# Kernel optimization log

Hardware: AMD Instinct MI355X
Metric: run time of the kernel (lower is better)

## Reference

```python
import jax, jax.numpy as jnp
import numpy as np

USER_NUM = 100000
ITEM_NUM = 50000
N_EDGES = 2000000
EMB = 64
N_LAYERS = 3


def setup_inputs() -> dict:
    key = jax.random.key(0)
    k1, k2, k3, k4 = jax.random.split(key, 4)
    # xavier-uniform-like init scale for embeddings
    scale = float(np.sqrt(6.0 / (USER_NUM + EMB)))
    user_emb = jax.random.uniform(k1, (USER_NUM, EMB), jnp.float32, -scale, scale)
    scale_i = float(np.sqrt(6.0 / (ITEM_NUM + EMB)))
    item_emb = jax.random.uniform(k2, (ITEM_NUM, EMB), jnp.float32, -scale_i, scale_i)
    u_idx = jax.random.randint(k3, (N_EDGES,), 0, USER_NUM, jnp.int32)
    i_idx = jax.random.randint(k4, (N_EDGES,), 0, ITEM_NUM, jnp.int32)
    return {"user_emb": user_emb, "item_emb": item_emb, "u_idx": u_idx, "i_idx": i_idx}


def _degree_norms(u_idx, i_idx):
    ones = jnp.ones(u_idx.shape[0], jnp.float32)
    d_u = jax.ops.segment_sum(ones, u_idx, num_segments=USER_NUM)
    d_i = jax.ops.segment_sum(ones, i_idx, num_segments=ITEM_NUM)
    d_u = jnp.where(d_u == 0, 1.0, d_u)
    d_i = jnp.where(d_i == 0, 1.0, d_i)
    return ((1.0 / d_u)[:, None], (1.0 / d_i)[:, None],
            (d_u ** -0.5)[:, None], (d_i ** -0.5)[:, None])


def reference(user_emb, item_emb, u_idx, i_idx):
    d_u_inv, d_i_inv, d_u_inv_sqrt, d_i_inv_sqrt = _degree_norms(u_idx, i_idx)

    # SpMM via gather + segment_sum on the edge list (binary interaction values)
    def spmm_rt(x_u):  # (rt @ x_u): [U,D] -> [I,D]
        return jax.ops.segment_sum(x_u[u_idx], i_idx, num_segments=ITEM_NUM)

    def spmm_r(x_i):  # (r @ x_i): [I,D] -> [U,D]
        return jax.ops.segment_sum(x_i[i_idx], u_idx, num_segments=USER_NUM)

    user_e = user_emb
    item_e = item_emb
    sum_u = user_e
    sum_i = item_e
    for _ in range(N_LAYERS):
        # user propagation: u -> hyperedge(items) -> u
        tmp_u = user_e * d_u_inv_sqrt
        tmp_i = spmm_rt(tmp_u) * d_i_inv
        user_e = spmm_r(tmp_i) * d_u_inv_sqrt
        sum_u = sum_u + user_e
        # item propagation: i -> hyperedge(users) -> i
        tmp_i2 = item_e * d_i_inv_sqrt
        tmp_u2 = spmm_r(tmp_i2) * d_u_inv
        item_e = spmm_rt(tmp_u2) * d_i_inv_sqrt
        sum_i = sum_i + item_e
    inv = 1.0 / (N_LAYERS + 1)
    return sum_u * inv, sum_i * inv
```

## Files before the change

### kernel.cpp

```cpp
#include <hip/hip_runtime.h>
#include <hip/hip_fp16.h>
#include <math.h>

#define U_NUM 100000
#define I_NUM 50000
#define NE    2000000
#define EMB   64
#define NLAYERS 3

#define BSH   7
#define BROWS 128
#define NBU_U ((U_NUM + BROWS - 1) >> BSH)
#define NBU_I ((I_NUM + BROWS - 1) >> BSH)
#define NBU_T (NBU_U + NBU_I)
#define PACK_SH 17
#define PACK_MASK 0x1FFFF

#define CAP_U 4096
#define CAP_I 6144

#define CHUNK2 2048
#define NBLK2 ((NE + CHUNK2 - 1) / CHUNK2)

#define DBINS 512

#define ND_U ((U_NUM + 2047) / 2048)
#define ND_I ((I_NUM + 2047) / 2048)
#define NINIT (((U_NUM + I_NUM) * (EMB / 4) + 255) / 256)

#define FP8_SCALE 512.0f

typedef float v2f __attribute__((ext_vector_type(2)));

static inline int ceil_div(int a, int b){ return (a + b - 1) / b; }


__global__ void binfill_k(const int* __restrict__ u_idx, const int* __restrict__ i_idx,
                          int* __restrict__ bcur_u, int* __restrict__ bcur_i,
                          int* __restrict__ bin_u, int* __restrict__ bin_i){
  __shared__ int scnt[NBU_T];
  __shared__ int gbase[NBU_T];
  __shared__ int scur[NBU_T];
  int t = threadIdx.x;
  for (int k = t; k < NBU_T; k += 256){ scnt[k] = 0; scur[k] = 0; }
  __syncthreads();
  int e0 = blockIdx.x * CHUNK2 + t * 8;
  int u[8], iv[8];
  bool act = e0 < NE;
  if (act){
    int4 a = *(const int4*)(u_idx + e0);
    int4 b = *(const int4*)(u_idx + e0 + 4);
    int4 c = *(const int4*)(i_idx + e0);
    int4 d = *(const int4*)(i_idx + e0 + 4);
    u[0]=a.x; u[1]=a.y; u[2]=a.z; u[3]=a.w; u[4]=b.x; u[5]=b.y; u[6]=b.z; u[7]=b.w;
    iv[0]=c.x; iv[1]=c.y; iv[2]=c.z; iv[3]=c.w; iv[4]=d.x; iv[5]=d.y; iv[6]=d.z; iv[7]=d.w;
#pragma unroll
    for (int k = 0; k < 8; ++k){
      atomicAdd(&scnt[u[k] >> BSH], 1);
      atomicAdd(&scnt[NBU_U + (iv[k] >> BSH)], 1);
    }
  }
  __syncthreads();
  for (int k = t; k < NBU_T; k += 256){
    int c = scnt[k];
    if (c){
      int* bc = (k < NBU_U) ? (bcur_u + k) : (bcur_i + (k - NBU_U));
      gbase[k] = atomicAdd(bc, c);
    }
  }
  __syncthreads();
  if (act){
#pragma unroll
    for (int k = 0; k < 8; ++k){
      int bu = u[k] >> BSH;
      int p = atomicAdd(&scur[bu], 1);
      bin_u[(size_t)bu * CAP_U + gbase[bu] + p] =
          ((u[k] & (BROWS - 1)) << PACK_SH) | iv[k];
      int bi = NBU_U + (iv[k] >> BSH);
      int p2 = atomicAdd(&scur[bi], 1);
      bin_i[(size_t)(bi - NBU_U) * CAP_I + gbase[bi] + p2] =
          ((iv[k] & (BROWS - 1)) << PACK_SH) | u[k];
    }
  }
}

__global__ void small_scan2_k(const int* __restrict__ cA, int* __restrict__ oA,
                              int* __restrict__ rA, int nA,
                              const int* __restrict__ cB, int* __restrict__ oB,
                              int* __restrict__ rB, int nB){
  const int* cnt; int* offs; int* cur; int n;
  if (blockIdx.x == 0){ cnt = cA; offs = oA; cur = rA; n = nA; }
  else { cnt = cB; offs = oB; cur = rB; n = nB; }
  __shared__ int s[1024];
  int t = threadIdx.x;
  int v = (t < n) ? cnt[t] : 0;
  s[t] = v; __syncthreads();
  for (int o = 1; o < 1024; o <<= 1){
    int x = (t >= o) ? s[t - o] : 0;
    __syncthreads();
    s[t] += x;
    __syncthreads();
  }
  int excl = (t > 0) ? s[t - 1] : 0;
  if (t < n){ offs[t] = excl; cur[t] = excl; }
  if (t == n - 1) offs[n] = s[t];
}


__global__ void bucket_build_k(const int* __restrict__ bin_u, const int* __restrict__ bin_i,
                               const int* __restrict__ bcnt_u, const int* __restrict__ bcnt_i,
                               const int* __restrict__ boffs_u, const int* __restrict__ boffs_i,
                               int* __restrict__ cnt_u, int* __restrict__ cnt_i,
                               int* __restrict__ offs_u, int* __restrict__ offs_i,
                               float* __restrict__ du_inv, float* __restrict__ du_invs,
                               float* __restrict__ di_inv, float* __restrict__ di_invs,
                               int* __restrict__ adj_u, int* __restrict__ adj_i,
                               int* __restrict__ dhist_u, int* __restrict__ dhist_i){
  __shared__ int h[BROWS];
  __shared__ int part[256];
  __shared__ int dh[DBINS];
  int b = blockIdx.x;
  const int* bin; const int* bcnt; const int* boffs; int* cnt; int* offs;
  float* inv; float* invs; int* adj; int* dhist; int jj, nrows; size_t cap;
  if (b < NBU_U){
    bin = bin_u; bcnt = bcnt_u; boffs = boffs_u; cnt = cnt_u; offs = offs_u;
    inv = du_inv; invs = du_invs; adj = adj_u; dhist = dhist_u; jj = b; nrows = U_NUM; cap = CAP_U;
  } else {
    bin = bin_i; bcnt = bcnt_i; boffs = boffs_i; cnt = cnt_i; offs = offs_i;
    inv = di_inv; invs = di_invs; adj = adj_i; dhist = dhist_i; jj = b - NBU_U; nrows = I_NUM; cap = CAP_I;
  }
  int tid = threadIdx.x;
  int r0 = jj << BSH;
  const int* binb = bin + (size_t)jj * cap;
  int ne = bcnt[jj];
  int badj = boffs[jj];
  if (tid < BROWS) h[tid] = 0;
  for (int t = tid; t < DBINS; t += 256) dh[t] = 0;
  __syncthreads();
  for (int e = tid; e < ne; e += 256)
    atomicAdd(&h[((unsigned)binb[e]) >> PACK_SH], 1);
  __syncthreads();
  int c = (tid < BROWS) ? h[tid] : 0;
  part[tid] = c; __syncthreads();
  for (int o = 1; o < 256; o <<= 1){
    int x = (tid >= o) ? part[tid - o] : 0;
    __syncthreads();
    part[tid] += x;
    __syncthreads();
  }
  int excl = (tid > 0) ? part[tid - 1] : 0;
  if (tid < BROWS){
    h[tid] = excl;
    int row = r0 + tid;
    if (row < nrows){
      cnt[row] = c;
      offs[row] = badj + excl;
      float d = (c > 0) ? (float)c : 1.0f;
      inv[row]  = 1.0f / d;
      invs[row] = 1.0f / sqrtf(d);
      atomicAdd(&dh[min(c, DBINS - 1)], 1);
    } else if (row == nrows){
      offs[row] = badj + excl;
    }
  }
  __syncthreads();
  for (int e = tid; e < ne; e += 256){
    int v = binb[e];
    int slot = badj + atomicAdd(&h[((unsigned)v) >> PACK_SH], 1);
    adj[slot] = v & PACK_MASK;
  }
  __syncthreads();
  for (int t = tid; t < DBINS; t += 256) if (dh[t]) atomicAdd(&dhist[t], dh[t]);
}


__device__ __forceinline__ unsigned pack4_fp8(float a, float b, float c, float d){
  int p = 0;
  p = __builtin_amdgcn_cvt_pk_fp8_f32(a, b, p, false);
  p = __builtin_amdgcn_cvt_pk_fp8_f32(c, d, p, true);
  return (unsigned)p;
}

__device__ __forceinline__ void accq(float* a, uint2 q){
  v2f f0 = __builtin_amdgcn_cvt_pk_f32_fp8(q.x, false);
  v2f f1 = __builtin_amdgcn_cvt_pk_f32_fp8(q.x, true);
  v2f f2 = __builtin_amdgcn_cvt_pk_f32_fp8(q.y, false);
  v2f f3 = __builtin_amdgcn_cvt_pk_f32_fp8(q.y, true);
  a[0] += f0.x; a[1] += f0.y; a[2] += f1.x; a[3] += f1.y;
  a[4] += f2.x; a[5] += f2.y; a[6] += f3.x; a[7] += f3.y;
}


__global__ void post_k(const int* __restrict__ cnt_u, const int* __restrict__ offs_u,
                       const int* __restrict__ dhist_u, int* __restrict__ dcur_u,
                       int4* __restrict__ rd_u,
                       const int* __restrict__ cnt_i, const int* __restrict__ offs_i,
                       const int* __restrict__ dhist_i, int* __restrict__ dcur_i,
                       int4* __restrict__ rd_i,
                       const float* __restrict__ ue, const float* __restrict__ ie,
                       const float* __restrict__ dus, const float* __restrict__ dis,
                       float* __restrict__ out, unsigned char* __restrict__ u0,
                       unsigned char* __restrict__ i0){
  int b = blockIdx.x;
  int t = threadIdx.x;
  if (b >= ND_U + ND_I){
    int idx4 = (b - ND_U - ND_I) * 256 + t;
    const int nu4 = U_NUM * (EMB / 4);
    const int tot4 = (U_NUM + I_NUM) * (EMB / 4);
    if (idx4 >= tot4) return;
    const float* e; unsigned char* hp; float s; int loc;
    if (idx4 < nu4){ e = ue; hp = u0; loc = idx4; s = dus[idx4 >> 4] * FP8_SCALE; }
    else { e = ie; hp = i0; loc = idx4 - nu4; s = dis[(idx4 - nu4) >> 4] * FP8_SCALE; }
    float4 v = ((const float4*)e)[loc];
    ((float4*)out)[idx4] = make_float4(v.x * 0.25f, v.y * 0.25f, v.z * 0.25f, v.w * 0.25f);
    ((unsigned*)hp)[loc] = pack4_fp8(v.x * s, v.y * s, v.z * s, v.w * s);
    return;
  }
  const int* cnt; const int* offs; const int* dhist; int* dcur; int4* rd; int n, base;
  if (b < ND_U){ cnt = cnt_u; offs = offs_u; dhist = dhist_u; dcur = dcur_u; rd = rd_u; n = U_NUM; base = b * 2048; }
  else { cnt = cnt_i; offs = offs_i; dhist = dhist_i; dcur = dcur_i; rd = rd_i; n = I_NUM; base = (b - ND_U) * 2048; }
  __shared__ int sc[DBINS];
  __shared__ int h[DBINS];
  __shared__ int base_s[DBINS];
  sc[t] = dhist[t]; sc[t + 256] = dhist[t + 256];
  h[t] = 0; h[t + 256] = 0;
  __syncthreads();
  for (int o = 1; o < DBINS; o <<= 1){
    int x0 = (t >= o) ? sc[t - o] : 0;
    int x1 = ((t + 256) >= o) ? sc[t + 256 - o] : 0;
    __syncthreads();
    sc[t] += x0; sc[t + 256] += x1;
    __syncthreads();
  }
  int end = min(base + 2048, n);
  for (int r = base + t; r < end; r += 256)
    atomicAdd(&h[min(cnt[r], DBINS - 1)], 1);
  __syncthreads();
  for (int tt = t; tt < DBINS; tt += 256){
    int c = h[tt];
    int excl = tt ? sc[tt - 1] : 0;
    base_s[tt] = c ? (excl + atomicAdd(&dcur[tt], c)) : 0;
    h[tt] = 0;
  }
  __syncthreads();
  for (int r = base + t; r < end; r += 256){
    int c = cnt[r];
    int bb = min(c, DBINS - 1);
    int pos = base_s[bb] + atomicAdd(&h[bb], 1);
    int bg = offs[r];
    rd[n - 1 - pos] = make_int4(bg, bg + c, r, 0);
  }
}


__global__ void spmm_pair(
    const int4* __restrict__ rdA, const int* __restrict__ adjA,
    const unsigned char* __restrict__ srcA, const float* __restrict__ phA,
    unsigned char* __restrict__ dstA, int nA,
    const int4* __restrict__ rdB, const int* __restrict__ adjB,
    const unsigned char* __restrict__ srcB, const float* __restrict__ phB,
    unsigned char* __restrict__ dstB, int nB){
  int t = blockIdx.x * blockDim.x + threadIdx.x;
  int rid = t >> 3;
  int lane = t & 7;
  const int4* rd; const int* adj; const unsigned char* src; const float* ph;
  unsigned char* dst;
  if (rid < nA){
    rd = rdA; adj = adjA; src = srcA; ph = phA; dst = dstA;
  } else {
    rid -= nA;
    if (rid >= nB) return;
    rd = rdB; adj = adjB; src = srcB; ph = phB; dst = dstB;
  }
  int4 d = rd[rid];
  int beg = d.x, end = d.y, row = d.z;
  const unsigned char* sp8 = src + (size_t)(lane << 3);
  float acc[8];
#pragma unroll
  for (int k = 0; k < 8; ++k) acc[k] = 0.f;
  int j = beg;
  for (; j + 7 < end; j += 8){
    int n0 = adj[j],   n1 = adj[j+1], n2 = adj[j+2], n3 = adj[j+3];
    int n4 = adj[j+4], n5 = adj[j+5], n6 = adj[j+6], n7 = adj[j+7];
    uint2 q0 = *(const uint2*)(sp8 + (((size_t)n0) << 6));
    uint2 q1 = *(const uint2*)(sp8 + (((size_t)n1) << 6));
    uint2 q2 = *(const uint2*)(sp8 + (((size_t)n2) << 6));
    uint2 q3 = *(const uint2*)(sp8 + (((size_t)n3) << 6));
    uint2 q4 = *(const uint2*)(sp8 + (((size_t)n4) << 6));
    uint2 q5 = *(const uint2*)(sp8 + (((size_t)n5) << 6));
    uint2 q6 = *(const uint2*)(sp8 + (((size_t)n6) << 6));
    uint2 q7 = *(const uint2*)(sp8 + (((size_t)n7) << 6));
    accq(acc, q0); accq(acc, q1); accq(acc, q2); accq(acc, q3);
    accq(acc, q4); accq(acc, q5); accq(acc, q6); accq(acc, q7);
  }
  for (; j < end; ++j){
    int n0 = adj[j];
    uint2 q0 = *(const uint2*)(sp8 + (((size_t)n0) << 6));
    accq(acc, q0);
  }
  float phv = ph[row];
  unsigned lo = pack4_fp8(acc[0] * phv, acc[1] * phv, acc[2] * phv, acc[3] * phv);
  unsigned hi = pack4_fp8(acc[4] * phv, acc[5] * phv, acc[6] * phv, acc[7] * phv);
  *(uint2*)(dst + (((size_t)row) << 6) + (size_t)(lane << 3)) = make_uint2(lo, hi);
}


__global__ void merge_k(const unsigned char* __restrict__ u1, const unsigned char* __restrict__ u2,
                        const unsigned char* __restrict__ u3,
                        const unsigned char* __restrict__ i1, const unsigned char* __restrict__ i2,
                        const unsigned char* __restrict__ i3,
                        const float* __restrict__ du_inv, const float* __restrict__ du_invs,
                        const float* __restrict__ di_inv, const float* __restrict__ di_invs,
                        float* __restrict__ out){
  int idx4 = blockIdx.x * blockDim.x + threadIdx.x;
  const int nu4 = U_NUM * (EMB / 4);
  const int tot4 = (U_NUM + I_NUM) * (EMB / 4);
  if (idx4 >= tot4) return;
  const unsigned char *t1, *t2, *t3; float ratio; int loc;
  if (idx4 < nu4){
    t1 = u1; t2 = u2; t3 = u3; loc = idx4;
    int row = idx4 >> 4;
    ratio = (0.25f / FP8_SCALE) * du_invs[row] / du_inv[row];
  } else {
    loc = idx4 - nu4;
    t1 = i1; t2 = i2; t3 = i3;
    int row = loc >> 4;
    ratio = (0.25f / FP8_SCALE) * di_invs[row] / di_inv[row];
  }
  unsigned q1 = ((const unsigned*)t1)[loc];
  unsigned q2 = ((const unsigned*)t2)[loc];
  unsigned q3 = ((const unsigned*)t3)[loc];
  float4 o = ((float4*)out)[idx4];
  v2f a, b;
  a = __builtin_amdgcn_cvt_pk_f32_fp8(q1, false); b = __builtin_amdgcn_cvt_pk_f32_fp8(q1, true);
  o.x += ratio * a.x; o.y += ratio * a.y; o.z += ratio * b.x; o.w += ratio * b.y;
  a = __builtin_amdgcn_cvt_pk_f32_fp8(q2, false); b = __builtin_amdgcn_cvt_pk_f32_fp8(q2, true);
  o.x += ratio * a.x; o.y += ratio * a.y; o.z += ratio * b.x; o.w += ratio * b.y;
  a = __builtin_amdgcn_cvt_pk_f32_fp8(q3, false); b = __builtin_amdgcn_cvt_pk_f32_fp8(q3, true);
  o.x += ratio * a.x; o.y += ratio * a.y; o.z += ratio * b.x; o.w += ratio * b.y;
  ((float4*)out)[idx4] = o;
}


extern "C" void kernel_launch(void* const* d_in, const int* in_sizes, int n_in,
                              void* d_out, int out_size, void* d_ws, size_t ws_size,
                              hipStream_t stream){
  const float* user_emb = (const float*)d_in[0];
  const float* item_emb = (const float*)d_in[1];
  const int*   u_idx    = (const int*)d_in[2];
  const int*   i_idx    = (const int*)d_in[3];
  float* out = (float*)d_out;

  char* w = (char*)d_ws;
  size_t off = 0;
  auto alloc = [&](size_t bytes) -> void* {
    void* p = (void*)(w + off);
    off += (bytes + 255) & ~(size_t)255;
    return p;
  };
  int* zb      = (int*)alloc((size_t)(NBU_T + 4 * DBINS) * 4);
  int* bcur_u  = zb;
  int* bcur_i  = bcur_u + NBU_U;
  int* dhist_u = bcur_i + NBU_I;
  int* dhist_i = dhist_u + DBINS;
  int* dcur_u  = dhist_i + DBINS;
  int* dcur_i  = dcur_u + DBINS;
  int* boffs_u = (int*)alloc((size_t)(NBU_U + 1) * 4);
  int* boffs_i = (int*)alloc((size_t)(NBU_I + 1) * 4);
  int* scr_u   = (int*)alloc((size_t)NBU_U * 4);
  int* scr_i   = (int*)alloc((size_t)NBU_I * 4);
  int* cnt_u   = (int*)alloc((size_t)U_NUM * 4);
  int* cnt_i   = (int*)alloc((size_t)I_NUM * 4);
  int* offs_u  = (int*)alloc((size_t)(U_NUM + 1) * 4);
  int* offs_i  = (int*)alloc((size_t)(I_NUM + 1) * 4);
  int4* rd_u   = (int4*)alloc((size_t)U_NUM * 16);
  int4* rd_i   = (int4*)alloc((size_t)I_NUM * 16);
  int* adj_u   = (int*)alloc((size_t)NE * 4);
  int* adj_i   = (int*)alloc((size_t)NE * 4);
  float* du_inv  = (float*)alloc((size_t)U_NUM * 4);
  float* du_invs = (float*)alloc((size_t)U_NUM * 4);
  float* di_inv  = (float*)alloc((size_t)I_NUM * 4);
  float* di_invs = (float*)alloc((size_t)I_NUM * 4);
  const size_t URB = (size_t)U_NUM * EMB;
  const size_t IRB = (size_t)I_NUM * EMB;
  unsigned char* hreg = (unsigned char*)alloc(4 * URB + 4 * IRB + URB + IRB);
  unsigned char* u0 = hreg;
  unsigned char* u1 = u0 + URB;
  unsigned char* u2 = u1 + URB;
  unsigned char* u3 = u2 + URB;
  unsigned char* i0 = u3 + URB;
  unsigned char* i1 = i0 + IRB;
  unsigned char* i2 = i1 + IRB;
  unsigned char* i3 = i2 + IRB;
  unsigned char* tmp_i = i3 + IRB;
  unsigned char* tmp_u = tmp_i + IRB;
  int* bin_u = (int*)hreg;
  int* bin_i = bin_u + (size_t)NBU_U * CAP_U;

  hipMemsetAsync(zb, 0, (size_t)(NBU_T + 4 * DBINS) * 4, stream);
  binfill_k<<<NBLK2, 256, 0, stream>>>(u_idx, i_idx, bcur_u, bcur_i, bin_u, bin_i);
  small_scan2_k<<<2, 1024, 0, stream>>>(bcur_u, boffs_u, scr_u, NBU_U,
                                        bcur_i, boffs_i, scr_i, NBU_I);
  bucket_build_k<<<NBU_T, 256, 0, stream>>>(bin_u, bin_i, bcur_u, bcur_i,
                                            boffs_u, boffs_i,
                                            cnt_u, cnt_i, offs_u, offs_i,
                                            du_inv, du_invs, di_inv, di_invs,
                                            adj_u, adj_i, dhist_u, dhist_i);

  post_k<<<ND_U + ND_I + NINIT, 256, 0, stream>>>(
      cnt_u, offs_u, dhist_u, dcur_u, rd_u,
      cnt_i, offs_i, dhist_i, dcur_i, rd_i,
      user_emb, item_emb, du_invs, di_invs, out, u0, i0);

  const int pair_grid = ceil_div((U_NUM + I_NUM) * 8, 256);
  unsigned char* uls[4] = { u0, u1, u2, u3 };
  unsigned char* ils[4] = { i0, i1, i2, i3 };
  for (int l = 0; l < NLAYERS; ++l){
    spmm_pair<<<pair_grid, 256, 0, stream>>>(
        rd_i, adj_i, uls[l], di_inv, tmp_i, I_NUM,
        rd_u, adj_u, ils[l], du_inv, tmp_u, U_NUM);
    spmm_pair<<<pair_grid, 256, 0, stream>>>(
        rd_u, adj_u, tmp_i, du_inv, uls[l + 1], U_NUM,
        rd_i, adj_i, tmp_u, di_inv, ils[l + 1], I_NUM);
  }

  merge_k<<<NINIT, 256, 0, stream>>>(u1, u2, u3, i1, i2, i3,
                                     du_inv, du_invs, di_inv, di_invs, out);
}
```

Baseline: 492.1 us.

## Widen SpMM gathers to 16-byte loads with four lanes per row, enlarge binfill chunks

The SpMM kernel now assigns four threads per row, each loading 16 fp8 values with a uint4 gather instead of eight threads each loading 8 bytes. This halves the thread count and gives wider memory transactions, at the cost of more registers per thread (16 accumulators) and less parallelism across rows. Separately, the binning kernel processes 8192 edges per block in a loop and re-reads the indices on the second pass. This is meant to amortize the per-block shared-memory init and the global atomics on bin cursors.

```diff
diff --git a/kernel.cpp b/kernel.cpp
--- a/kernel.cpp
+++ b/kernel.cpp
@@ -19,7 +19,7 @@
 #define CAP_U 4096
 #define CAP_I 6144
 
-#define CHUNK2 2048
+#define CHUNK2 8192
 #define NBLK2 ((NE + CHUNK2 - 1) / CHUNK2)
 
 #define DBINS 512
@@ -44,21 +44,21 @@
   int t = threadIdx.x;
   for (int k = t; k < NBU_T; k += 256){ scnt[k] = 0; scur[k] = 0; }
   __syncthreads();
-  int e0 = blockIdx.x * CHUNK2 + t * 8;
-  int u[8], iv[8];
-  bool act = e0 < NE;
-  if (act){
+  int base = blockIdx.x * CHUNK2;
+  int end = min(base + CHUNK2, NE);
+  for (int e0 = base + t * 8; e0 < end; e0 += 2048){
     int4 a = *(const int4*)(u_idx + e0);
     int4 b = *(const int4*)(u_idx + e0 + 4);
     int4 c = *(const int4*)(i_idx + e0);
     int4 d = *(const int4*)(i_idx + e0 + 4);
-    u[0]=a.x; u[1]=a.y; u[2]=a.z; u[3]=a.w; u[4]=b.x; u[5]=b.y; u[6]=b.z; u[7]=b.w;
-    iv[0]=c.x; iv[1]=c.y; iv[2]=c.z; iv[3]=c.w; iv[4]=d.x; iv[5]=d.y; iv[6]=d.z; iv[7]=d.w;
-#pragma unroll
-    for (int k = 0; k < 8; ++k){
-      atomicAdd(&scnt[u[k] >> BSH], 1);
-      atomicAdd(&scnt[NBU_U + (iv[k] >> BSH)], 1);
-    }
+    atomicAdd(&scnt[a.x >> BSH], 1); atomicAdd(&scnt[a.y >> BSH], 1);
+    atomicAdd(&scnt[a.z >> BSH], 1); atomicAdd(&scnt[a.w >> BSH], 1);
+    atomicAdd(&scnt[b.x >> BSH], 1); atomicAdd(&scnt[b.y >> BSH], 1);
+    atomicAdd(&scnt[b.z >> BSH], 1); atomicAdd(&scnt[b.w >> BSH], 1);
+    atomicAdd(&scnt[NBU_U + (c.x >> BSH)], 1); atomicAdd(&scnt[NBU_U + (c.y >> BSH)], 1);
+    atomicAdd(&scnt[NBU_U + (c.z >> BSH)], 1); atomicAdd(&scnt[NBU_U + (c.w >> BSH)], 1);
+    atomicAdd(&scnt[NBU_U + (d.x >> BSH)], 1); atomicAdd(&scnt[NBU_U + (d.y >> BSH)], 1);
+    atomicAdd(&scnt[NBU_U + (d.z >> BSH)], 1); atomicAdd(&scnt[NBU_U + (d.w >> BSH)], 1);
   }
   __syncthreads();
   for (int k = t; k < NBU_T; k += 256){
@@ -69,7 +69,13 @@
     }
   }
   __syncthreads();
-  if (act){
+  for (int e0 = base + t * 8; e0 < end; e0 += 2048){
+    int4 a = *(const int4*)(u_idx + e0);
+    int4 b = *(const int4*)(u_idx + e0 + 4);
+    int4 c = *(const int4*)(i_idx + e0);
+    int4 d = *(const int4*)(i_idx + e0 + 4);
+    int u[8] = { a.x, a.y, a.z, a.w, b.x, b.y, b.z, b.w };
+    int iv[8] = { c.x, c.y, c.z, c.w, d.x, d.y, d.z, d.w };
 #pragma unroll
     for (int k = 0; k < 8; ++k){
       int bu = u[k] >> BSH;
@@ -181,13 +187,14 @@
   return (unsigned)p;
 }
 
-__device__ __forceinline__ void accq(float* a, uint2 q){
-  v2f f0 = __builtin_amdgcn_cvt_pk_f32_fp8(q.x, false);
-  v2f f1 = __builtin_amdgcn_cvt_pk_f32_fp8(q.x, true);
-  v2f f2 = __builtin_amdgcn_cvt_pk_f32_fp8(q.y, false);
-  v2f f3 = __builtin_amdgcn_cvt_pk_f32_fp8(q.y, true);
+__device__ __forceinline__ void accw(float* a, unsigned w){
+  v2f f0 = __builtin_amdgcn_cvt_pk_f32_fp8(w, false);
+  v2f f1 = __builtin_amdgcn_cvt_pk_f32_fp8(w, true);
   a[0] += f0.x; a[1] += f0.y; a[2] += f1.x; a[3] += f1.y;
-  a[4] += f2.x; a[5] += f2.y; a[6] += f3.x; a[7] += f3.y;
+}
+
+__device__ __forceinline__ void accq16(float* a, uint4 q){
+  accw(a, q.x); accw(a + 4, q.y); accw(a + 8, q.z); accw(a + 12, q.w);
 }
 
 
@@ -261,8 +268,8 @@
     const unsigned char* __restrict__ srcB, const float* __restrict__ phB,
     unsigned char* __restrict__ dstB, int nB){
   int t = blockIdx.x * blockDim.x + threadIdx.x;
-  int rid = t >> 3;
-  int lane = t & 7;
+  int rid = t >> 2;
+  int lane = t & 3;
   const int4* rd; const int* adj; const unsigned char* src; const float* ph;
   unsigned char* dst;
   if (rid < nA){
@@ -274,34 +281,37 @@
   }
   int4 d = rd[rid];
   int beg = d.x, end = d.y, row = d.z;
-  const unsigned char* sp8 = src + (size_t)(lane << 3);
-  float acc[8];
+  const unsigned char* sp16 = src + (size_t)(lane << 4);
+  float acc[16];
 #pragma unroll
-  for (int k = 0; k < 8; ++k) acc[k] = 0.f;
+  for (int k = 0; k < 16; ++k) acc[k] = 0.f;
   int j = beg;
   for (; j + 7 < end; j += 8){
     int n0 = adj[j],   n1 = adj[j+1], n2 = adj[j+2], n3 = adj[j+3];
     int n4 = adj[j+4], n5 = adj[j+5], n6 = adj[j+6], n7 = adj[j+7];
-    uint2 q0 = *(const uint2*)(sp8 + (((size_t)n0) << 6));
-    uint2 q1 = *(const uint2*)(sp8 + (((size_t)n1) << 6));
-    uint2 q2 = *(const uint2*)(sp8 + (((size_t)n2) << 6));
-    uint2 q3 = *(const uint2*)(sp8 + (((size_t)n3) << 6));
-    uint2 q4 = *(const uint2*)(sp8 + (((size_t)n4) << 6));
-    uint2 q5 = *(const uint2*)(sp8 + (((size_t)n5) << 6));
-    uint2 q6 = *(const uint2*)(sp8 + (((size_t)n6) << 6));
-    uint2 q7 = *(const uint2*)(sp8 + (((size_t)n7) << 6));
-    accq(acc, q0); accq(acc, q1); accq(acc, q2); accq(acc, q3);
-    accq(acc, q4); accq(acc, q5); accq(acc, q6); accq(acc, q7);
+    uint4 q0 = *(const uint4*)(sp16 + (((size_t)n0) << 6));
+    uint4 q1 = *(const uint4*)(sp16 + (((size_t)n1) << 6));
+    uint4 q2 = *(const uint4*)(sp16 + (((size_t)n2) << 6));
+    uint4 q3 = *(const uint4*)(sp16 + (((size_t)n3) << 6));
+    uint4 q4 = *(const uint4*)(sp16 + (((size_t)n4) << 6));
+    uint4 q5 = *(const uint4*)(sp16 + (((size_t)n5) << 6));
+    uint4 q6 = *(const uint4*)(sp16 + (((size_t)n6) << 6));
+    uint4 q7 = *(const uint4*)(sp16 + (((size_t)n7) << 6));
+    accq16(acc, q0); accq16(acc, q1); accq16(acc, q2); accq16(acc, q3);
+    accq16(acc, q4); accq16(acc, q5); accq16(acc, q6); accq16(acc, q7);
   }
   for (; j < end; ++j){
     int n0 = adj[j];
-    uint2 q0 = *(const uint2*)(sp8 + (((size_t)n0) << 6));
-    accq(acc, q0);
+    uint4 q0 = *(const uint4*)(sp16 + (((size_t)n0) << 6));
+    accq16(acc, q0);
   }
   float phv = ph[row];
-  unsigned lo = pack4_fp8(acc[0] * phv, acc[1] * phv, acc[2] * phv, acc[3] * phv);
-  unsigned hi = pack4_fp8(acc[4] * phv, acc[5] * phv, acc[6] * phv, acc[7] * phv);
-  *(uint2*)(dst + (((size_t)row) << 6) + (size_t)(lane << 3)) = make_uint2(lo, hi);
+  uint4 o;
+  o.x = pack4_fp8(acc[0] * phv,  acc[1] * phv,  acc[2] * phv,  acc[3] * phv);
+  o.y = pack4_fp8(acc[4] * phv,  acc[5] * phv,  acc[6] * phv,  acc[7] * phv);
+  o.z = pack4_fp8(acc[8] * phv,  acc[9] * phv,  acc[10] * phv, acc[11] * phv);
+  o.w = pack4_fp8(acc[12] * phv, acc[13] * phv, acc[14] * phv, acc[15] * phv);
+  *(uint4*)(dst + (((size_t)row) << 6) + (size_t)(lane << 4)) = o;
 }
 
 
@@ -412,7 +422,7 @@
       cnt_i, offs_i, dhist_i, dcur_i, rd_i,
       user_emb, item_emb, du_invs, di_invs, out, u0, i0);
 
-  const int pair_grid = ceil_div((U_NUM + I_NUM) * 8, 256);
+  const int pair_grid = ceil_div((U_NUM + I_NUM) * 4, 256);
   unsigned char* uls[4] = { u0, u1, u2, u3 };
   unsigned char* ils[4] = { i0, i1, i2, i3 };
   for (int l = 0; l < NLAYERS; ++l){
```

Result: slower. 959.4 us (+95.0%).
